# Kernel tuning notes

Measured on AMD Instinct MI355X. Metric: run time of the kernel, lower is better.

The kernel has to match this reference:

```python
import jax, jax.numpy as jnp
import numpy as np

N, FIN, F, H = 4096, 128, 64, 8
NEG = -1e10


def setup_inputs() -> dict:
    key = jax.random.key(0)
    ks = jax.random.split(key, 6)
    X = jax.random.normal(ks[0], (N, FIN), dtype=jnp.float32)
    # sparse-ish binary adjacency with self loops, stored dense (as the layer expects)
    A = (jax.random.uniform(ks[1], (N, N)) < 0.05).astype(jnp.int32)
    A = A.at[jnp.arange(N), jnp.arange(N)].set(1)
    W = jax.random.normal(ks[2], (H, FIN, F), dtype=jnp.float32) * (1.0 / np.sqrt(FIN))
    b = jnp.zeros((H, F), dtype=jnp.float32)
    a_self = jax.random.normal(ks[3], (H, F), dtype=jnp.float32) * (1.0 / np.sqrt(F))
    a_neigh = jax.random.normal(ks[4], (H, F), dtype=jnp.float32) * (1.0 / np.sqrt(F))
    return {"X": X, "A": A, "W": W, "b": b, "a_self": a_self, "a_neigh": a_neigh}


def reference(X, A, W, b, a_self, a_neigh):
    # Dropout layers run in inference mode in the original call -> identity.
    feats = jnp.einsum('nf,hfo->hno', X, W)              # [H, N, F]
    s_self = jnp.einsum('hno,ho->hn', feats, a_self)     # [H, N]
    s_neigh = jnp.einsum('hno,ho->hn', feats, a_neigh)   # [H, N]
    scores = s_self[:, :, None] + s_neigh[:, None, :]    # [H, N, N]
    scores = jnp.where(scores > 0, scores, 0.2 * scores)  # LeakyReLU(0.2)
    mask = (1.0 - A.astype(jnp.float32)) * NEG            # [N, N]
    attn = jax.nn.softmax(scores + mask[None], axis=-1)   # [H, N, N]
    out = jnp.einsum('hnm,hmo->hno', attn, feats) + b[:, None, :]
    out = jax.nn.elu(out)                                 # [H, N, F]
    # concat heads -> [N, H*F]
    return jnp.transpose(out, (1, 0, 2)).reshape(N, H * F)
```

## Files before the change

kernel.cpp:

```cpp
#include <hip/hip_runtime.h>
#include <cmath>


#define NN 4096
#define FIN 128
#define FF 64
#define HH 8

typedef _Float16 h2 __attribute__((ext_vector_type(2)));
typedef _Float16 h8 __attribute__((ext_vector_type(8)));
typedef _Float16 half4 __attribute__((ext_vector_type(4)));
typedef float f32x4 __attribute__((ext_vector_type(4)));

union H8 {
  h8 v;
  h2 p[4];
};

static __device__ __forceinline__ float dot2acc(h2 a, h2 b, float c) {
#if __has_builtin(__builtin_amdgcn_fdot2)
  return __builtin_amdgcn_fdot2(a, b, c, false);
#else
  return c + (float)a[0] * (float)b[0] + (float)a[1] * (float)b[1];
#endif
}

__global__ __launch_bounds__(256) void pack_kernel(
    const int* __restrict__ A, unsigned long long* __restrict__ bits) {
  const int row = blockIdx.x;
  const int wave = threadIdx.x >> 6, lane = threadIdx.x & 63;
  const int* ar = A + (size_t)row * NN;
  for (int w = wave; w < 64; w += 4) {
    int v = ar[(w << 6) + lane];
    unsigned long long m = __ballot(v != 0);
    if (lane == 0) bits[(row << 6) + w] = m;
  }
}

__global__ __launch_bounds__(256) void feats_kernel(
    const float* __restrict__ X, const float* __restrict__ W,
    const float* __restrict__ a_self, const float* __restrict__ a_neigh,
    _Float16* __restrict__ feats_sw, _Float16* __restrict__ es_h,
    _Float16* __restrict__ esn_h, _Float16* __restrict__ et_h,
    _Float16* __restrict__ etn_h) {
  const int h = blockIdx.y, r0 = blockIdx.x * 64;
  __shared__ float Wl[128][68];
  __shared__ float Xl[64][68];
  const int tid = threadIdx.x, tx = tid & 15, ty = tid >> 4;

  f32x4 acc4[4];
#pragma unroll
  for (int i = 0; i < 4; ++i) acc4[i] = (f32x4){0.f, 0.f, 0.f, 0.f};

  for (int idx = tid; idx < 128 * 16; idx += 256) {
    int k = idx >> 4, c4 = (idx & 15) << 2;
    *(f32x4*)&Wl[k][c4] = *(const f32x4*)(W + (size_t)(h * FIN + k) * FF + c4);
  }
  for (int p = 0; p < 2; ++p) {
    __syncthreads();
    for (int idx = tid; idx < 64 * 16; idx += 256) {
      int r = idx >> 4, c4 = (idx & 15) << 2;
      *(f32x4*)&Xl[r][c4] =
          *(const f32x4*)(X + (size_t)(r0 + r) * FIN + p * 64 + c4);
    }
    __syncthreads();
    for (int kk = 0; kk < 64; ++kk) {
      f32x4 wv = *(const f32x4*)&Wl[p * 64 + kk][tx << 2];
#pragma unroll
      for (int i = 0; i < 4; ++i) {
        float x = Xl[(ty << 2) + i][kk];
        acc4[i] += x * wv;
      }
    }
  }

  float as4[4], an4[4];
#pragma unroll
  for (int jj = 0; jj < 4; ++jj) {
    as4[jj] = a_self[h * FF + (tx << 2) + jj];
    an4[jj] = a_neigh[h * FF + (tx << 2) + jj];
  }
#pragma unroll
  for (int i = 0; i < 4; ++i) {
    float ps = acc4[i][0] * as4[0] + acc4[i][1] * as4[1] +
               acc4[i][2] * as4[2] + acc4[i][3] * as4[3];
    float pn = acc4[i][0] * an4[0] + acc4[i][1] * an4[1] +
               acc4[i][2] * an4[2] + acc4[i][3] * an4[3];
#pragma unroll
    for (int m = 1; m <= 8; m <<= 1) {
      ps += __shfl_xor(ps, m, 64);
      pn += __shfl_xor(pn, m, 64);
    }
    if (tx == 0) {
      int node = h * NN + r0 + (ty << 2) + i;
      es_h[node] = (_Float16)__expf(ps - 2.0f);
      esn_h[node] = (_Float16)__expf(0.2f * ps - 2.0f);
      et_h[node] = (_Float16)__expf(pn - 2.0f);
      etn_h[node] = (_Float16)__expf(0.2f * pn - 2.0f);
    }
  }

  const int kb = (r0 + (ty << 2)) >> 5;
  const int quad = (ty >> 1) & 3;
  const int jbase = (ty & 1) << 2;
  const int nb = tx >> 2;
#pragma unroll
  for (int jj = 0; jj < 4; ++jj) {
    half4 v;
#pragma unroll
    for (int i = 0; i < 4; ++i) v[i] = (_Float16)acc4[i][jj];
    int l16 = ((tx & 3) << 2) + jj;
    size_t off = ((size_t)((h * 128 + kb) * 4 + nb) << 9) +
                 ((quad * 16 + l16) << 3) + jbase;
    *(half4*)(feats_sw + off) = v;
  }
}

__global__ __launch_bounds__(256, 2) void attn_kernel(
    const unsigned long long* __restrict__ Abits,
    const _Float16* __restrict__ feats_sw, const _Float16* __restrict__ es_h,
    const _Float16* __restrict__ esn_h, const _Float16* __restrict__ et_h,
    const _Float16* __restrict__ etn_h, const float* __restrict__ bias,
    float* __restrict__ out) {
  const int bid = blockIdx.x;
  const int h = bid & 7, rb = bid >> 3;
  const int n0 = rb << 6;
  const int tid = threadIdx.x, wave = tid >> 6, lane = tid & 63;
  const int l16 = lane & 15, quad = lane >> 4;

  __shared__ h8 lut[256];
  __shared__ float accL[4][32][66];
  __shared__ float denL[4][64];
  {
    h8 m;
#pragma unroll
    for (int j = 0; j < 8; ++j) m[j] = (_Float16)((tid >> j) & 1);
    lut[tid] = m;
  }
  __syncthreads();

  h2 esp[4], esnp[4];
#pragma unroll
  for (int rg = 0; rg < 4; ++rg) {
    _Float16 e = es_h[h * NN + n0 + rg * 16 + l16];
    _Float16 en = esn_h[h * NN + n0 + rg * 16 + l16];
    esp[rg] = (h2){e, e};
    esnp[rg] = (h2){en, en};
  }

  f32x4 acc[4][4];
  float dsum[4] = {0.f, 0.f, 0.f, 0.f};
#pragma unroll
  for (int rg = 0; rg < 4; ++rg)
#pragma unroll
    for (int nb = 0; nb < 4; ++nb) acc[rg][nb] = (f32x4){0.f, 0.f, 0.f, 0.f};

  const uint2* ab = (const uint2*)Abits;
  const int rowbase = n0 + l16;
  const _Float16* etp = et_h + h * NN + (quad << 3);
  const _Float16* etnp = etn_h + h * NN + (quad << 3);
  const _Float16* fb = feats_sw + ((size_t)h << 18) + (lane << 3);

  for (int ct = wave; ct < 64; ct += 4) {
    uint2 bits[4];
#pragma unroll
    for (int rg = 0; rg < 4; ++rg)
      bits[rg] = ab[((rowbase + rg * 16) << 6) + ct];
    const _Float16* fbt = fb + (ct << 12);
#pragma unroll
    for (int kf = 0; kf < 2; ++kf) {
      H8 ET, ETN;
      ET.v = *(const h8*)(etp + (ct << 6) + kf * 32);
      ETN.v = *(const h8*)(etnp + (ct << 6) + kf * 32);
      const _Float16* fk = fbt + (kf << 11);
      h8 B0 = *(const h8*)(fk);
      h8 B1 = *(const h8*)(fk + 512);
      h8 B2 = *(const h8*)(fk + 1024);
      h8 B3 = *(const h8*)(fk + 1536);
#pragma unroll
      for (int rg = 0; rg < 4; ++rg) {
        unsigned word = kf ? bits[rg].y : bits[rg].x;
        unsigned byt = (word >> (quad << 3)) & 0xFFu;
        H8 mm;
        mm.v = lut[byt];
        H8 P;
#pragma unroll
        for (int p = 0; p < 4; ++p) {
          h2 a = esp[rg] * ET.p[p];
          h2 b = esnp[rg] * ETN.p[p];
          h2 r = __builtin_elementwise_max(a, b);
          h2 pm = r * mm.p[p];
          P.p[p] = pm;
          dsum[rg] = dot2acc(pm, (h2){(_Float16)1.f, (_Float16)1.f}, dsum[rg]);
        }
        acc[rg][0] =
            __builtin_amdgcn_mfma_f32_16x16x32_f16(P.v, B0, acc[rg][0], 0, 0, 0);
        acc[rg][1] =
            __builtin_amdgcn_mfma_f32_16x16x32_f16(P.v, B1, acc[rg][1], 0, 0, 0);
        acc[rg][2] =
            __builtin_amdgcn_mfma_f32_16x16x32_f16(P.v, B2, acc[rg][2], 0, 0, 0);
        acc[rg][3] =
            __builtin_amdgcn_mfma_f32_16x16x32_f16(P.v, B3, acc[rg][3], 0, 0, 0);
      }
    }
  }

#pragma unroll
  for (int rg = 0; rg < 4; ++rg) {
    float d = dsum[rg];
    d += __shfl_xor(d, 16, 64);
    d += __shfl_xor(d, 32, 64);
    if (quad == 0) denL[wave][rg * 16 + l16] = d;
  }

  const int lrow = tid >> 3, cgg = (tid & 7) << 3;
#pragma unroll
  for (int ph = 0; ph < 2; ++ph) {
    __syncthreads();
#pragma unroll
    for (int rg2 = 0; rg2 < 2; ++rg2) {
      int rg = ph * 2 + rg2;
#pragma unroll
      for (int nb = 0; nb < 4; ++nb)
#pragma unroll
        for (int r = 0; r < 4; ++r)
          accL[wave][rg2 * 16 + quad * 4 + r][nb * 16 + l16] = acc[rg][nb][r];
    }
    __syncthreads();
    const int row = ph * 32 + lrow;
    float dn = denL[0][row] + denL[1][row] + denL[2][row] + denL[3][row];
    float inv = 1.0f / dn;
    f32x4 r0, r1;
#pragma unroll
    for (int i = 0; i < 4; ++i) {
      r0[i] = accL[0][lrow][cgg + i] + accL[1][lrow][cgg + i] +
              accL[2][lrow][cgg + i] + accL[3][lrow][cgg + i];
      r1[i] = accL[0][lrow][cgg + 4 + i] + accL[1][lrow][cgg + 4 + i] +
              accL[2][lrow][cgg + 4 + i] + accL[3][lrow][cgg + 4 + i];
    }
    const f32x4 b0 = *(const f32x4*)(bias + h * FF + cgg);
    const f32x4 b1 = *(const f32x4*)(bias + h * FF + cgg + 4);
#pragma unroll
    for (int i = 0; i < 4; ++i) {
      float v0 = r0[i] * inv + b0[i];
      float v1 = r1[i] * inv + b1[i];
      r0[i] = v0 > 0.f ? v0 : expm1f(v0);
      r1[i] = v1 > 0.f ? v1 : expm1f(v1);
    }
    float* op = out + (size_t)(n0 + row) * (HH * FF) + h * FF + cgg;
    *(f32x4*)op = r0;
    *(f32x4*)(op + 4) = r1;
  }
}

extern "C" void kernel_launch(void* const* d_in, const int* in_sizes, int n_in,
                              void* d_out, int out_size, void* d_ws,
                              size_t ws_size, hipStream_t stream) {
  const float* X = (const float*)d_in[0];
  const int* A = (const int*)d_in[1];
  const float* W = (const float*)d_in[2];
  const float* b = (const float*)d_in[3];
  const float* a_self = (const float*)d_in[4];
  const float* a_neigh = (const float*)d_in[5];
  float* out = (float*)d_out;

  char* ws = (char*)d_ws;
  unsigned long long* Abits = (unsigned long long*)ws;
  _Float16* feats_sw = (_Float16*)(ws + (2u << 20));
  _Float16* es_h = (_Float16*)(ws + (6u << 20));
  _Float16* esn_h = (_Float16*)(ws + (6u << 20) + (64u << 10));
  _Float16* et_h = (_Float16*)(ws + (6u << 20) + (128u << 10));
  _Float16* etn_h = (_Float16*)(ws + (6u << 20) + (192u << 10));

  pack_kernel<<<NN, 256, 0, stream>>>(A, Abits);
  feats_kernel<<<dim3(64, 8), 256, 0, stream>>>(X, W, a_self, a_neigh,
                                                feats_sw, es_h, esn_h, et_h,
                                                etn_h);
  attn_kernel<<<512, 256, 0, stream>>>(Abits, feats_sw, es_h, esn_h, et_h,
                                       etn_h, b, out);
}
```

Baseline: 170.3 us.

## Use MFMA for feature projection, widen attention blocks, unroll adjacency packing

Rewrites the feature projection to convert X and W to fp16 and compute with MFMA instead of fp32 FMA, processing 128 rows per block. Attention blocks grow to 512 threads (8 waves split the column tiles) with a smaller 16-entry mask LUT, and the epilogue reduces over 8 partial accumulators. The pack kernel unrolls four ballots per iteration for more loads in flight. The trade-offs are fp16 rounding of X and W, a larger shared-memory reduction in attention, and a less accurate expf-based ELU.

```diff
diff --git a/kernel.cpp b/kernel.cpp
--- a/kernel.cpp
+++ b/kernel.cpp
@@ -8,20 +8,25 @@
 #define HH 8
 
 typedef _Float16 h2 __attribute__((ext_vector_type(2)));
+typedef _Float16 h4 __attribute__((ext_vector_type(4)));
 typedef _Float16 h8 __attribute__((ext_vector_type(8)));
-typedef _Float16 half4 __attribute__((ext_vector_type(4)));
 typedef float f32x4 __attribute__((ext_vector_type(4)));
 
 union H8 {
   h8 v;
   h2 p[4];
 };
-
-static __device__ __forceinline__ float dot2acc(h2 a, h2 b, float c) {
+union H4 {
+  h4 v;
+  h2 p[2];
+};
+
+static __device__ __forceinline__ float dot2acc(h2 a, float c) {
 #if __has_builtin(__builtin_amdgcn_fdot2)
-  return __builtin_amdgcn_fdot2(a, b, c, false);
+  return __builtin_amdgcn_fdot2(a, (h2){(_Float16)1.f, (_Float16)1.f}, c,
+                                false);
 #else
-  return c + (float)a[0] * (float)b[0] + (float)a[1] * (float)b[1];
+  return c + (float)a[0] + (float)a[1];
 #endif
 }
 
@@ -30,10 +35,23 @@
   const int row = blockIdx.x;
   const int wave = threadIdx.x >> 6, lane = threadIdx.x & 63;
   const int* ar = A + (size_t)row * NN;
-  for (int w = wave; w < 64; w += 4) {
-    int v = ar[(w << 6) + lane];
-    unsigned long long m = __ballot(v != 0);
-    if (lane == 0) bits[(row << 6) + w] = m;
+#pragma unroll
+  for (int g = 0; g < 4; ++g) {
+    const int w0 = wave * 16 + g * 4;
+    int v0 = ar[(w0 + 0) * 64 + lane];
+    int v1 = ar[(w0 + 1) * 64 + lane];
+    int v2 = ar[(w0 + 2) * 64 + lane];
+    int v3 = ar[(w0 + 3) * 64 + lane];
+    unsigned long long m0 = __ballot(v0 != 0);
+    unsigned long long m1 = __ballot(v1 != 0);
+    unsigned long long m2 = __ballot(v2 != 0);
+    unsigned long long m3 = __ballot(v3 != 0);
+    if (lane == 0) {
+      bits[(row << 6) + w0 + 0] = m0;
+      bits[(row << 6) + w0 + 1] = m1;
+      bits[(row << 6) + w0 + 2] = m2;
+      bits[(row << 6) + w0 + 3] = m3;
+    }
   }
 }
 
@@ -43,99 +61,110 @@
     _Float16* __restrict__ feats_sw, _Float16* __restrict__ es_h,
     _Float16* __restrict__ esn_h, _Float16* __restrict__ et_h,
     _Float16* __restrict__ etn_h) {
-  const int h = blockIdx.y, r0 = blockIdx.x * 64;
-  __shared__ float Wl[128][68];
-  __shared__ float Xl[64][68];
-  const int tid = threadIdx.x, tx = tid & 15, ty = tid >> 4;
-
-  f32x4 acc4[4];
-#pragma unroll
-  for (int i = 0; i < 4; ++i) acc4[i] = (f32x4){0.f, 0.f, 0.f, 0.f};
-
-  for (int idx = tid; idx < 128 * 16; idx += 256) {
-    int k = idx >> 4, c4 = (idx & 15) << 2;
-    *(f32x4*)&Wl[k][c4] = *(const f32x4*)(W + (size_t)(h * FIN + k) * FF + c4);
-  }
-  for (int p = 0; p < 2; ++p) {
-    __syncthreads();
-    for (int idx = tid; idx < 64 * 16; idx += 256) {
-      int r = idx >> 4, c4 = (idx & 15) << 2;
-      *(f32x4*)&Xl[r][c4] =
-          *(const f32x4*)(X + (size_t)(r0 + r) * FIN + p * 64 + c4);
-    }
-    __syncthreads();
-    for (int kk = 0; kk < 64; ++kk) {
-      f32x4 wv = *(const f32x4*)&Wl[p * 64 + kk][tx << 2];
-#pragma unroll
-      for (int i = 0; i < 4; ++i) {
-        float x = Xl[(ty << 2) + i][kk];
-        acc4[i] += x * wv;
+  const int h = blockIdx.y, r0 = blockIdx.x * 128;
+  const int tid = threadIdx.x, wave = tid >> 6, lane = tid & 63;
+  const int l16 = lane & 15, quad = lane >> 4;
+
+  __shared__ _Float16 Xh[128][136];
+  __shared__ _Float16 Wt[64][136];
+
+  for (int i = tid; i < 128 * 32; i += 256) {
+    int row = i >> 5, c4 = (i & 31) << 2;
+    f32x4 x = *(const f32x4*)(X + (size_t)(r0 + row) * FIN + c4);
+    h4 hx = {(_Float16)x[0], (_Float16)x[1], (_Float16)x[2], (_Float16)x[3]};
+    *(h4*)&Xh[row][c4] = hx;
+  }
+  for (int i = tid; i < 128 * 16; i += 256) {
+    int k = i >> 4, f4 = (i & 15) << 2;
+    f32x4 w = *(const f32x4*)(W + (size_t)(h * FIN + k) * FF + f4);
+#pragma unroll
+    for (int j = 0; j < 4; ++j) Wt[f4 + j][k] = (_Float16)w[j];
+  }
+  __syncthreads();
+
+  f32x4 acc[2][4];
+#pragma unroll
+  for (int rg = 0; rg < 2; ++rg)
+#pragma unroll
+    for (int nb = 0; nb < 4; ++nb) acc[rg][nb] = (f32x4){0.f, 0.f, 0.f, 0.f};
+
+#pragma unroll
+  for (int kt = 0; kt < 4; ++kt) {
+    const int kof = kt * 32 + quad * 8;
+    h8 A0 = *(const h8*)&Xh[wave * 32 + l16][kof];
+    h8 A1 = *(const h8*)&Xh[wave * 32 + 16 + l16][kof];
+#pragma unroll
+    for (int nb = 0; nb < 4; ++nb) {
+      h8 B = *(const h8*)&Wt[nb * 16 + l16][kof];
+      acc[0][nb] = __builtin_amdgcn_mfma_f32_16x16x32_f16(A0, B, acc[0][nb], 0, 0, 0);
+      acc[1][nb] = __builtin_amdgcn_mfma_f32_16x16x32_f16(A1, B, acc[1][nb], 0, 0, 0);
+    }
+  }
+
+  float as[4], an[4];
+#pragma unroll
+  for (int nb = 0; nb < 4; ++nb) {
+    as[nb] = a_self[h * FF + nb * 16 + l16];
+    an[nb] = a_neigh[h * FF + nb * 16 + l16];
+  }
+#pragma unroll
+  for (int rg = 0; rg < 2; ++rg)
+#pragma unroll
+    for (int r = 0; r < 4; ++r) {
+      float ps = acc[rg][0][r] * as[0] + acc[rg][1][r] * as[1] +
+                 acc[rg][2][r] * as[2] + acc[rg][3][r] * as[3];
+      float pn = acc[rg][0][r] * an[0] + acc[rg][1][r] * an[1] +
+                 acc[rg][2][r] * an[2] + acc[rg][3][r] * an[3];
+#pragma unroll
+      for (int m = 1; m <= 8; m <<= 1) {
+        ps += __shfl_xor(ps, m, 64);
+        pn += __shfl_xor(pn, m, 64);
       }
-    }
-  }
-
-  float as4[4], an4[4];
-#pragma unroll
-  for (int jj = 0; jj < 4; ++jj) {
-    as4[jj] = a_self[h * FF + (tx << 2) + jj];
-    an4[jj] = a_neigh[h * FF + (tx << 2) + jj];
-  }
-#pragma unroll
-  for (int i = 0; i < 4; ++i) {
-    float ps = acc4[i][0] * as4[0] + acc4[i][1] * as4[1] +
-               acc4[i][2] * as4[2] + acc4[i][3] * as4[3];
-    float pn = acc4[i][0] * an4[0] + acc4[i][1] * an4[1] +
-               acc4[i][2] * an4[2] + acc4[i][3] * an4[3];
-#pragma unroll
-    for (int m = 1; m <= 8; m <<= 1) {
-      ps += __shfl_xor(ps, m, 64);
-      pn += __shfl_xor(pn, m, 64);
-    }
-    if (tx == 0) {
-      int node = h * NN + r0 + (ty << 2) + i;
-      es_h[node] = (_Float16)__expf(ps - 2.0f);
-      esn_h[node] = (_Float16)__expf(0.2f * ps - 2.0f);
-      et_h[node] = (_Float16)__expf(pn - 2.0f);
-      etn_h[node] = (_Float16)__expf(0.2f * pn - 2.0f);
-    }
-  }
-
-  const int kb = (r0 + (ty << 2)) >> 5;
-  const int quad = (ty >> 1) & 3;
-  const int jbase = (ty & 1) << 2;
-  const int nb = tx >> 2;
-#pragma unroll
-  for (int jj = 0; jj < 4; ++jj) {
-    half4 v;
-#pragma unroll
-    for (int i = 0; i < 4; ++i) v[i] = (_Float16)acc4[i][jj];
-    int l16 = ((tx & 3) << 2) + jj;
-    size_t off = ((size_t)((h * 128 + kb) * 4 + nb) << 9) +
-                 ((quad * 16 + l16) << 3) + jbase;
-    *(half4*)(feats_sw + off) = v;
-  }
-}
-
-__global__ __launch_bounds__(256, 2) void attn_kernel(
+      if (l16 == 0) {
+        int node = h * NN + r0 + wave * 32 + rg * 16 + quad * 4 + r;
+        es_h[node] = (_Float16)__expf(ps - 2.0f);
+        esn_h[node] = (_Float16)__expf(0.2f * ps - 2.0f);
+        et_h[node] = (_Float16)__expf(pn - 2.0f);
+        etn_h[node] = (_Float16)__expf(0.2f * pn - 2.0f);
+      }
+    }
+
+  const int kb = (r0 >> 5) + wave;
+  const int quad2base = quad >> 1;
+  const int jbase = (quad & 1) << 2;
+#pragma unroll
+  for (int rg = 0; rg < 2; ++rg) {
+    const int quad2 = rg * 2 + quad2base;
+#pragma unroll
+    for (int nb = 0; nb < 4; ++nb) {
+      h4 v = {(_Float16)acc[rg][nb][0], (_Float16)acc[rg][nb][1],
+              (_Float16)acc[rg][nb][2], (_Float16)acc[rg][nb][3]};
+      size_t off = ((size_t)((h * 128 + kb) * 4 + nb) << 9) +
+                   ((quad2 * 16 + l16) << 3) + jbase;
+      *(h4*)(feats_sw + off) = v;
+    }
+  }
+}
+
+__global__ __launch_bounds__(512, 4) void attn_kernel(
     const unsigned long long* __restrict__ Abits,
     const _Float16* __restrict__ feats_sw, const _Float16* __restrict__ es_h,
     const _Float16* __restrict__ esn_h, const _Float16* __restrict__ et_h,
     const _Float16* __restrict__ etn_h, const float* __restrict__ bias,
     float* __restrict__ out) {
   const int bid = blockIdx.x;
-  const int h = bid & 7, rb = bid >> 3;
-  const int n0 = rb << 6;
+  const int h = bid & 7, n0 = (bid >> 3) << 6;
   const int tid = threadIdx.x, wave = tid >> 6, lane = tid & 63;
   const int l16 = lane & 15, quad = lane >> 4;
 
-  __shared__ h8 lut[256];
-  __shared__ float accL[4][32][66];
-  __shared__ float denL[4][64];
-  {
-    h8 m;
-#pragma unroll
-    for (int j = 0; j < 8; ++j) m[j] = (_Float16)((tid >> j) & 1);
-    lut[tid] = m;
+  __shared__ h4 lut16[16];
+  __shared__ float accL[8][32][66];
+  __shared__ float denL[8][64];
+  if (tid < 16) {
+    h4 m;
+#pragma unroll
+    for (int j = 0; j < 4; ++j) m[j] = (_Float16)((tid >> j) & 1);
+    lut16[tid] = m;
   }
   __syncthreads();
 
@@ -161,7 +190,7 @@
   const _Float16* etnp = etn_h + h * NN + (quad << 3);
   const _Float16* fb = feats_sw + ((size_t)h << 18) + (lane << 3);
 
-  for (int ct = wave; ct < 64; ct += 4) {
+  for (int ct = wave; ct < 64; ct += 8) {
     uint2 bits[4];
 #pragma unroll
     for (int rg = 0; rg < 4; ++rg)
@@ -181,17 +210,18 @@
       for (int rg = 0; rg < 4; ++rg) {
         unsigned word = kf ? bits[rg].y : bits[rg].x;
         unsigned byt = (word >> (quad << 3)) & 0xFFu;
-        H8 mm;
-        mm.v = lut[byt];
+        H4 mlo, mhi;
+        mlo.v = lut16[byt & 15u];
+        mhi.v = lut16[byt >> 4];
         H8 P;
 #pragma unroll
         for (int p = 0; p < 4; ++p) {
           h2 a = esp[rg] * ET.p[p];
           h2 b = esnp[rg] * ETN.p[p];
           h2 r = __builtin_elementwise_max(a, b);
-          h2 pm = r * mm.p[p];
+          h2 pm = r * (p < 2 ? mlo.p[p] : mhi.p[p - 2]);
           P.p[p] = pm;
-          dsum[rg] = dot2acc(pm, (h2){(_Float16)1.f, (_Float16)1.f}, dsum[rg]);
+          dsum[rg] = dot2acc(pm, dsum[rg]);
         }
         acc[rg][0] =
             __builtin_amdgcn_mfma_f32_16x16x32_f16(P.v, B0, acc[rg][0], 0, 0, 0);
@@ -213,7 +243,7 @@
     if (quad == 0) denL[wave][rg * 16 + l16] = d;
   }
 
-  const int lrow = tid >> 3, cgg = (tid & 7) << 3;
+  const int erow = tid >> 4, ec0 = (tid & 15) << 2;
 #pragma unroll
   for (int ph = 0; ph < 2; ++ph) {
     __syncthreads();
@@ -227,29 +257,25 @@
           accL[wave][rg2 * 16 + quad * 4 + r][nb * 16 + l16] = acc[rg][nb][r];
     }
     __syncthreads();
-    const int row = ph * 32 + lrow;
-    float dn = denL[0][row] + denL[1][row] + denL[2][row] + denL[3][row];
+    const int grow = ph * 32 + erow;
+    float dn = 0.f;
+#pragma unroll
+    for (int w = 0; w < 8; ++w) dn += denL[w][grow];
     float inv = 1.0f / dn;
-    f32x4 r0, r1;
+    f32x4 v = (f32x4){0.f, 0.f, 0.f, 0.f};
+#pragma unroll
+    for (int w = 0; w < 8; ++w) {
+      f32x4 t = *(const f32x4*)&accL[w][erow][ec0];
+      v += t;
+    }
+    const f32x4 bv = *(const f32x4*)(bias + h * FF + ec0);
 #pragma unroll
     for (int i = 0; i < 4; ++i) {
-      r0[i] = accL[0][lrow][cgg + i] + accL[1][lrow][cgg + i] +
-              accL[2][lrow][cgg + i] + accL[3][lrow][cgg + i];
-      r1[i] = accL[0][lrow][cgg + 4 + i] + accL[1][lrow][cgg + 4 + i] +
-              accL[2][lrow][cgg + 4 + i] + accL[3][lrow][cgg + 4 + i];
-    }
-    const f32x4 b0 = *(const f32x4*)(bias + h * FF + cgg);
-    const f32x4 b1 = *(const f32x4*)(bias + h * FF + cgg + 4);
-#pragma unroll
-    for (int i = 0; i < 4; ++i) {
-      float v0 = r0[i] * inv + b0[i];
-      float v1 = r1[i] * inv + b1[i];
-      r0[i] = v0 > 0.f ? v0 : expm1f(v0);
-      r1[i] = v1 > 0.f ? v1 : expm1f(v1);
-    }
-    float* op = out + (size_t)(n0 + row) * (HH * FF) + h * FF + cgg;
-    *(f32x4*)op = r0;
-    *(f32x4*)(op + 4) = r1;
+      float x = v[i] * inv + bv[i];
+      v[i] = x > 0.f ? x : (__expf(x) - 1.0f);
+    }
+    float* op = out + (size_t)(n0 + grow) * (HH * FF) + h * FF + ec0;
+    *(f32x4*)op = v;
   }
 }
 
@@ -273,9 +299,9 @@
   _Float16* etn_h = (_Float16*)(ws + (6u << 20) + (192u << 10));
 
   pack_kernel<<<NN, 256, 0, stream>>>(A, Abits);
-  feats_kernel<<<dim3(64, 8), 256, 0, stream>>>(X, W, a_self, a_neigh,
+  feats_kernel<<<dim3(32, 8), 256, 0, stream>>>(X, W, a_self, a_neigh,
                                                 feats_sw, es_h, esn_h, et_h,
                                                 etn_h);
-  attn_kernel<<<512, 256, 0, stream>>>(Abits, feats_sw, es_h, esn_h, et_h,
+  attn_kernel<<<512, 512, 0, stream>>>(Abits, feats_sw, es_h, esn_h, et_h,
                                        etn_h, b, out);
 }
```

Measured after the change: 152.5 us. 1.12x faster.
